# Kernel tuning notes

Hardware: AMD Instinct MI355X
Metric: run time of the kernel (lower is better)

Reference implementation:

```python
import jax, jax.numpy as jnp
import numpy as np

NUM_HEADS = 16
HEAD_DIM = 64
MAX_TIME = 10000


def apply_rope(x):
    """Interleaved RoPE, faithful to apply_rotary_encoding with the _rope_kernel.

    The NxN kernel maps pairs (x0, x1) -> (-x1, x0); we do it with a reshape
    instead of the dense matmul for efficiency (same math).
    x: [b, t, h, d]
    """
    b, t, h, d = x.shape
    pos = jnp.arange(t, dtype=jnp.float32)                         # [t]
    freq_seq = jnp.arange(d // 2, dtype=jnp.float32) / (d // 2)
    inv_freq = jnp.repeat(jnp.float32(MAX_TIME) ** (-freq_seq), 2)  # [d], interleaved
    theta = pos[:, None] * inv_freq[None, :]                        # [t, d]
    pairs = x.reshape(b, t, h, d // 2, 2)
    x_rot = jnp.stack([-pairs[..., 1], pairs[..., 0]], axis=-1).reshape(b, t, h, d)
    cos = jnp.cos(theta).astype(x.dtype)[None, :, None, :]
    sin = jnp.sin(theta).astype(x.dtype)[None, :, None, :]
    return x * cos + x_rot * sin


def setup_inputs() -> dict:
    key = jax.random.key(0)
    ks = jax.random.split(key, 6)
    B, T, E = 8, 1024, 1024
    H = NUM_HEADS * HEAD_DIM
    s = 0.02  # typical init scale for bias-free Linear weights
    return {
        "inputs_q": jax.random.normal(ks[0], (B, T, E), jnp.float32),
        "inputs_kv": jax.random.normal(ks[1], (B, T, E), jnp.float32),
        "w_q": jax.random.normal(ks[2], (E, H), jnp.float32) * s,
        "w_k": jax.random.normal(ks[3], (E, H), jnp.float32) * s,
        "w_v": jax.random.normal(ks[4], (E, H), jnp.float32) * s,
        "w_o": jax.random.normal(ks[5], (H, E), jnp.float32) * s,
    }


def reference(inputs_q, inputs_kv, w_q, w_k, w_v, w_o):
    b, t, e = inputs_q.shape
    q = (inputs_q @ w_q).reshape(b, t, NUM_HEADS, HEAD_DIM)   # [b,t,h,d]
    k = (inputs_kv @ w_k).reshape(b, -1, NUM_HEADS, HEAD_DIM)  # [b,T,h,d]
    v = (inputs_kv @ w_v).reshape(b, -1, NUM_HEADS, HEAD_DIM)
    q = apply_rope(q)
    k = apply_rope(k)
    logits = jnp.einsum('bthd,bThd->bhtT', q, k) * (1.0 / jnp.sqrt(jnp.float32(HEAD_DIM)))
    attn = jax.nn.softmax(logits, axis=-1)                    # [b,h,t,T]
    out = jnp.einsum('bhtT,bThd->bthd', attn, v).reshape(b, t, NUM_HEADS * HEAD_DIM)
    return out @ w_o                                          # [b,t,e]
```

## Files before the change

### kernel.cpp

```cpp
#include <hip/hip_runtime.h>
#include <math.h>


typedef __attribute__((ext_vector_type(8))) short bf16x8;
typedef __attribute__((ext_vector_type(4))) float f32x4;
typedef __attribute__((ext_vector_type(16))) float f32x16;

#define LOG2E 1.44269504f
#define QSCALE (0.125f * LOG2E)

__device__ __forceinline__ ushort f2bf(float f) {
    union { float f; uint32_t u; } v; v.f = f;
    uint32_t r = (v.u + 0x7FFF + ((v.u >> 16) & 1)) >> 16;
    return (ushort)r;
}
__device__ __forceinline__ uint cvt_pk_bf16(float a, float b) {
    uint r;
    asm("v_cvt_pk_bf16_f32 %0, %1, %2" : "=v"(r) : "v"(a), "v"(b));
    return r;
}
__device__ __forceinline__ float bf2f(ushort u) {
    union { uint32_t u; float f; } v; v.u = ((uint32_t)u) << 16;
    return v.f;
}

__device__ __forceinline__ void gload16(const ushort* g, ushort* l) {
    __builtin_amdgcn_global_load_lds(
        (const __attribute__((address_space(1))) unsigned int*)g,
        (__attribute__((address_space(3))) unsigned int*)l, 16, 0, 0);
}

__global__ void build_rope_tbl(float2* __restrict__ tbl)
{
    int idx = blockIdx.x * 256 + threadIdx.x;
    int t = idx >> 5, i = idx & 31;
    float inv_freq = exp2f(-(float)i * (13.28771238f / 32.0f));
    float s, c;
    sincosf((float)t * inv_freq, &s, &c);
    tbl[idx] = make_float2(c, s);
}

__global__ void cast_bf16_2(const float* __restrict__ X0, ushort* __restrict__ Y0,
                            const float* __restrict__ X1, ushort* __restrict__ Y1)
{
    const float* X = blockIdx.y ? X1 : X0;
    ushort* Y = blockIdx.y ? Y1 : Y0;
    int i = blockIdx.x * 256 + threadIdx.x;
    float4 a = ((const float4*)X)[2 * i];
    float4 b = ((const float4*)X)[2 * i + 1];
    union { float4 f; ushort u[8]; } o;
    o.u[0] = f2bf(a.x); o.u[1] = f2bf(a.y); o.u[2] = f2bf(a.z); o.u[3] = f2bf(a.w);
    o.u[4] = f2bf(b.x); o.u[5] = f2bf(b.y); o.u[6] = f2bf(b.z); o.u[7] = f2bf(b.w);
    ((float4*)Y)[i] = o.f;
}

__global__ void transpose_cast_4(const float* __restrict__ w0, ushort* __restrict__ t0,
                                 const float* __restrict__ w1, ushort* __restrict__ t1,
                                 const float* __restrict__ w2, ushort* __restrict__ t2,
                                 const float* __restrict__ w3, ushort* __restrict__ t3)
{
    const int z = blockIdx.z;
    const float* W = (z == 0) ? w0 : (z == 1) ? w1 : (z == 2) ? w2 : w3;
    ushort* Wt = (z == 0) ? t0 : (z == 1) ? t1 : (z == 2) ? t2 : t3;
    __shared__ float t[32][33];
    int bx = blockIdx.x * 32, by = blockIdx.y * 32;
    int tx = threadIdx.x, ty = threadIdx.y;
#pragma unroll
    for (int e = 0; e < 32; e += 8)
        t[ty + e][tx] = W[(size_t)(by + ty + e) * 1024 + bx + tx];
    __syncthreads();
#pragma unroll
    for (int e = 0; e < 32; e += 8)
        Wt[(size_t)(bx + ty + e) * 1024 + by + tx] = f2bf(t[tx][ty + e]);
}

__global__ __launch_bounds__(256, 4)
void gemm_qkv(const ushort* __restrict__ Aq, const ushort* __restrict__ Akv,
              const ushort* __restrict__ Wt, ushort* __restrict__ Out,
              const float2* __restrict__ tbl)
{
    const int K = 1024, N = 1024;
    __shared__ ushort As[2][128 * 32];
    __shared__ ushort Bs[2][128 * 32];
    const int tid = threadIdx.x;
    const int w = tid >> 6, l = tid & 63;
    const int mat = blockIdx.y >> 3;
    const int row0 = blockIdx.x * 128, col0 = (blockIdx.y & 7) * 128;
    const int wr = (w >> 1) * 64, wc = (w & 1) * 64;

    const ushort* A = mat ? Akv : Aq;
    const ushort* Bt = Wt + (size_t)mat * (1024 * 1024);
    ushort* C = Out + (size_t)mat * 8388608;

    f32x4 acc[4][4];
#pragma unroll
    for (int i = 0; i < 4; ++i)
#pragma unroll
        for (int j = 0; j < 4; ++j) acc[i][j] = (f32x4)0.f;

    const ushort* Ag = A + (size_t)(row0 + w * 32 + (l >> 2)) * K + (l & 3) * 8;
    const ushort* Bg = Bt + (size_t)(col0 + w * 32 + (l >> 2)) * K + (l & 3) * 8;

    const int arow = (wr + (l & 15)) * 32;
    const int brow = (wc + (l & 15)) * 32;
    const int koff = (l >> 4) * 8;

    auto STAGE = [&](int buf, int kt) {
        ushort* Asw = &As[buf][w * 1024];
        ushort* Bsw = &Bs[buf][w * 1024];
        gload16(Ag + kt, Asw);
        gload16(Ag + 16 * K + kt, Asw + 512);
        gload16(Bg + kt, Bsw);
        gload16(Bg + 16 * K + kt, Bsw + 512);
    };
    auto COMPUTE = [&](int buf) {
        bf16x8 af[4], bfr[4];
#pragma unroll
        for (int fm = 0; fm < 4; ++fm)
            af[fm] = *(const bf16x8*)&As[buf][arow + fm * 512 + koff];
#pragma unroll
        for (int fn = 0; fn < 4; ++fn)
            bfr[fn] = *(const bf16x8*)&Bs[buf][brow + fn * 512 + koff];
#pragma unroll
        for (int fm = 0; fm < 4; ++fm)
#pragma unroll
            for (int fn = 0; fn < 4; ++fn)
                acc[fm][fn] = __builtin_amdgcn_mfma_f32_16x16x32_bf16(
                    af[fm], bfr[fn], acc[fm][fn], 0, 0, 0);
    };

    STAGE(0, 0);
    asm volatile("s_waitcnt vmcnt(0)" ::: "memory");
    __builtin_amdgcn_s_barrier();
    int cur = 0;
    for (int kt = 32; kt < K; kt += 32) {
        STAGE(cur ^ 1, kt);
        COMPUTE(cur);
        asm volatile("s_waitcnt vmcnt(0)" ::: "memory");
        __builtin_amdgcn_s_barrier();
        cur ^= 1;
    }
    COMPUTE(cur);

    const int crow = (l >> 4) * 4;
    const int ccol = l & 15;

    if (mat < 2) {
        const float scale = (mat == 0) ? QSCALE : 1.0f;
        const int odd = ccol & 1;
        int ipair[4];
#pragma unroll
        for (int fn = 0; fn < 4; ++fn)
            ipair[fn] = (fn * 16 + ccol) >> 1;
#pragma unroll
        for (int fm = 0; fm < 4; ++fm)
#pragma unroll
            for (int r = 0; r < 4; ++r) {
                int t = (row0 + wr + fm * 16 + crow + r) & 1023;
                const float2* tb = tbl + (t << 5);
#pragma unroll
                for (int fn = 0; fn < 4; ++fn) {
                    float x = acc[fm][fn][r];
                    float partner = __shfl_xor(x, 1, 64);
                    float2 cs = tb[ipair[fn]];
                    float o = odd ? fmaf(partner, cs.y, x * cs.x)
                                  : fmaf(-partner, cs.y, x * cs.x);
                    acc[fm][fn][r] = o * scale;
                }
            }
    }

#pragma unroll
    for (int fm = 0; fm < 4; ++fm)
#pragma unroll
        for (int fn = 0; fn < 4; ++fn)
#pragma unroll
            for (int r = 0; r < 4; ++r) {
                size_t row = row0 + wr + fm * 16 + crow + r;
                size_t col = col0 + wc + fn * 16 + ccol;
                C[row * N + col] = f2bf(acc[fm][fn][r]);
            }
}

__global__ __launch_bounds__(256, 2)
void gemm_out(const ushort* __restrict__ A, const ushort* __restrict__ Bt,
              float* __restrict__ C, int M, int N, int K)
{
    __shared__ ushort As[2][128 * 32];
    __shared__ ushort Bs[2][128 * 32];
    const int tid = threadIdx.x;
    const int w = tid >> 6, l = tid & 63;
    const int row0 = blockIdx.x * 128, col0 = blockIdx.y * 128;
    const int wr = (w >> 1) * 64, wc = (w & 1) * 64;

    f32x4 acc[4][4];
#pragma unroll
    for (int i = 0; i < 4; ++i)
#pragma unroll
        for (int j = 0; j < 4; ++j) acc[i][j] = (f32x4)0.f;

    const ushort* Ag = A + (size_t)(row0 + w * 32 + (l >> 2)) * K + (l & 3) * 8;
    const ushort* Bg = Bt + (size_t)(col0 + w * 32 + (l >> 2)) * K + (l & 3) * 8;

    const int arow = (wr + (l & 15)) * 32;
    const int brow = (wc + (l & 15)) * 32;
    const int koff = (l >> 4) * 8;

    auto STAGE = [&](int buf, int kt) {
        ushort* Asw = &As[buf][w * 1024];
        ushort* Bsw = &Bs[buf][w * 1024];
        gload16(Ag + kt, Asw);
        gload16(Ag + 16 * K + kt, Asw + 512);
        gload16(Bg + kt, Bsw);
        gload16(Bg + 16 * K + kt, Bsw + 512);
    };
    auto COMPUTE = [&](int buf) {
        bf16x8 af[4], bfr[4];
#pragma unroll
        for (int fm = 0; fm < 4; ++fm)
            af[fm] = *(const bf16x8*)&As[buf][arow + fm * 512 + koff];
#pragma unroll
        for (int fn = 0; fn < 4; ++fn)
            bfr[fn] = *(const bf16x8*)&Bs[buf][brow + fn * 512 + koff];
#pragma unroll
        for (int fm = 0; fm < 4; ++fm)
#pragma unroll
            for (int fn = 0; fn < 4; ++fn)
                acc[fm][fn] = __builtin_amdgcn_mfma_f32_16x16x32_bf16(
                    af[fm], bfr[fn], acc[fm][fn], 0, 0, 0);
    };

    STAGE(0, 0);
    asm volatile("s_waitcnt vmcnt(0)" ::: "memory");
    __builtin_amdgcn_s_barrier();
    int cur = 0;
    for (int kt = 32; kt < K; kt += 32) {
        STAGE(cur ^ 1, kt);
        COMPUTE(cur);
        asm volatile("s_waitcnt vmcnt(0)" ::: "memory");
        __builtin_amdgcn_s_barrier();
        cur ^= 1;
    }
    COMPUTE(cur);

    const int crow = (l >> 4) * 4;
    const int ccol = l & 15;
#pragma unroll
    for (int fm = 0; fm < 4; ++fm)
#pragma unroll
        for (int fn = 0; fn < 4; ++fn)
#pragma unroll
            for (int r = 0; r < 4; ++r) {
                size_t row = row0 + wr + fm * 16 + crow + r;
                size_t col = col0 + wc + fn * 16 + ccol;
                C[row * N + col] = acc[fm][fn][r];
            }
}

__global__ __launch_bounds__(256, 4)
void attn_bf16_v2(const ushort* __restrict__ Q, const ushort* __restrict__ K,
                  const ushort* __restrict__ V, ushort* __restrict__ O)
{
    __shared__ uint Ksu[64 * 34];
    __shared__ uint Vtu[64 * 34];
    __shared__ uint Os[4][32 * 36];

    const int tid = threadIdx.x;
    const int w = tid >> 6, l = tid & 63;
    const int lo = l & 31, hi = l >> 5;
    const int bid = blockIdx.x;
    const int qt = bid >> 7;
    const int hb = bid & 127;
    const int h = hb >> 3, b = hb & 7;
    const int colh = h * 64;

    const size_t qrow = (size_t)(b * 1024 + qt * 128 + w * 32 + lo);
    bf16x8 qb[4];
#pragma unroll
    for (int kc = 0; kc < 4; ++kc)
        qb[kc] = *(const bf16x8*)&Q[qrow * 1024 + colh + kc * 16 + hi * 8];

    f32x16 acc[2];
#pragma unroll
    for (int i = 0; i < 2; ++i) acc[i] = (f32x16)0.f;
    float lsum = 0.f;

    const size_t kvbase = (size_t)b * 1024 * 1024 + colh;

    const int skey = tid >> 3, sc = tid & 7;
    const int kp = tid & 31, vg = tid >> 5;

    for (int kt = 0; kt < 16; ++kt) {
        __syncthreads();
#pragma unroll
        for (int u = 0; u < 2; ++u) {
            int key = skey + u * 32;
            uint4 kv = *(const uint4*)&K[kvbase + (size_t)(kt * 64 + key) * 1024 + sc * 8];
            *(uint2*)&Ksu[key * 34 + sc * 4] = make_uint2(kv.x, kv.y);
            *(uint2*)&Ksu[key * 34 + sc * 4 + 2] = make_uint2(kv.z, kv.w);
        }
        {
            uint4 va = *(const uint4*)&V[kvbase + (size_t)(kt * 64 + 2 * kp) * 1024 + vg * 8];
            uint4 vb = *(const uint4*)&V[kvbase + (size_t)(kt * 64 + 2 * kp + 1) * 1024 + vg * 8];
            const ushort* pa = (const ushort*)&va;
            const ushort* pb = (const ushort*)&vb;
#pragma unroll
            for (int e = 0; e < 8; ++e)
                Vtu[(vg * 8 + e) * 34 + kp] = (uint)pa[e] | ((uint)pb[e] << 16);
        }
        __syncthreads();

        uint pw[16];
#pragma unroll
        for (int mt = 0; mt < 2; ++mt) {
            f32x16 s = (f32x16)0.f;
            const int rbase = (mt * 32 + lo) * 34 + hi * 4;
#pragma unroll
            for (int kc = 0; kc < 4; ++kc) {
                union { uint2 d[2]; bf16x8 v; } ak;
                ak.d[0] = *(const uint2*)&Ksu[rbase + kc * 8];
                ak.d[1] = *(const uint2*)&Ksu[rbase + kc * 8 + 2];
                s = __builtin_amdgcn_mfma_f32_32x32x16_bf16(ak.v, qb[kc], s, 0, 0, 0);
            }
            float p[16];
#pragma unroll
            for (int r = 0; r < 16; ++r) {
                p[r] = exp2f(s[r]);
                lsum += p[r];
            }
#pragma unroll
            for (int rp = 0; rp < 8; ++rp)
                pw[mt * 8 + rp] = cvt_pk_bf16(p[2 * rp], p[2 * rp + 1]);
        }

        bf16x8 pf[4];
#pragma unroll
        for (int mt = 0; mt < 2; ++mt) {
            uint* W = &pw[mt * 8];
            uint e0 = (uint)__shfl_xor((int)(hi ? W[0] : W[2]), 32);
            uint e1 = (uint)__shfl_xor((int)(hi ? W[1] : W[3]), 32);
            uint e2 = (uint)__shfl_xor((int)(hi ? W[4] : W[6]), 32);
            uint e3 = (uint)__shfl_xor((int)(hi ? W[5] : W[7]), 32);
            union { uint u[4]; bf16x8 v; } f0, f1;
            if (hi == 0) {
                f0.u[0] = W[0]; f0.u[1] = W[1]; f0.u[2] = e0; f0.u[3] = e1;
                f1.u[0] = W[4]; f1.u[1] = W[5]; f1.u[2] = e2; f1.u[3] = e3;
            } else {
                f0.u[0] = e0; f0.u[1] = e1; f0.u[2] = W[2]; f0.u[3] = W[3];
                f1.u[0] = e2; f1.u[1] = e3; f1.u[2] = W[6]; f1.u[3] = W[7];
            }
            pf[mt * 2 + 0] = f0.v;
            pf[mt * 2 + 1] = f1.v;
        }

#pragma unroll
        for (int dmt = 0; dmt < 2; ++dmt) {
            const int rbase = (dmt * 32 + lo) * 34 + hi * 4;
#pragma unroll
            for (int kcg = 0; kcg < 4; ++kcg) {
                union { uint2 d[2]; bf16x8 v; } vk;
                vk.d[0] = *(const uint2*)&Vtu[rbase + kcg * 8];
                vk.d[1] = *(const uint2*)&Vtu[rbase + kcg * 8 + 2];
                acc[dmt] = __builtin_amdgcn_mfma_f32_32x32x16_bf16(vk.v, pf[kcg], acc[dmt], 0, 0, 0);
            }
        }
    }

    float tot = lsum + __shfl_xor(lsum, 32);
    float inv = 1.0f / tot;

    uint* Osw = &Os[w][0];
#pragma unroll
    for (int dmt = 0; dmt < 2; ++dmt)
#pragma unroll
        for (int rp = 0; rp < 8; ++rp) {
            float a0 = acc[dmt][2 * rp] * inv;
            float a1 = acc[dmt][2 * rp + 1] * inv;
            Osw[lo * 36 + dmt * 16 + (rp & 1) + 4 * (rp >> 1) + 2 * hi] =
                cvt_pk_bf16(a0, a1);
        }
    __builtin_amdgcn_s_waitcnt(0);
#pragma unroll
    for (int u = 0; u < 4; ++u) {
        int slot = l + u * 64;
        int qr = slot >> 3, c = slot & 7;
        float4 val = *(const float4*)&Osw[qr * 36 + c * 4];
        *(float4*)&O[(size_t)(b * 1024 + qt * 128 + w * 32 + qr) * 1024 + colh + c * 8] = val;
    }
}

extern "C" void kernel_launch(void* const* d_in, const int* in_sizes, int n_in,
                              void* d_out, int out_size, void* d_ws, size_t ws_size,
                              hipStream_t stream)
{
    const float* xq  = (const float*)d_in[0];
    const float* xkv = (const float*)d_in[1];
    const float* wq  = (const float*)d_in[2];
    const float* wk  = (const float*)d_in[3];
    const float* wv  = (const float*)d_in[4];
    const float* wo  = (const float*)d_in[5];
    float* out = (float*)d_out;

    const int M = 8192, N = 1024, Kd = 1024;
    ushort* Aq  = (ushort*)d_ws;
    ushort* Akv = Aq  + 8388608;
    ushort* WqT = Akv + 8388608;
    ushort* WkT = WqT + 1048576;
    ushort* WvT = WkT + 1048576;
    ushort* WoT = WvT + 1048576;
    ushort* Qb  = WoT + 1048576;
    ushort* Kb  = Qb  + 8388608;
    ushort* Vb  = Kb  + 8388608;
    ushort* Ob  = Vb  + 8388608;
    float2* Tbl = (float2*)(Ob + 8388608);

    build_rope_tbl<<<128, 256, 0, stream>>>(Tbl);
    cast_bf16_2<<<dim3(4096, 2), 256, 0, stream>>>(xq, Aq, xkv, Akv);
    transpose_cast_4<<<dim3(32, 32, 4), dim3(32, 8), 0, stream>>>(
        wq, WqT, wk, WkT, wv, WvT, wo, WoT);

    gemm_qkv<<<dim3(64, 24), 256, 0, stream>>>(Aq, Akv, WqT, Qb, Tbl);

    attn_bf16_v2<<<1024, 256, 0, stream>>>(Qb, Kb, Vb, Ob);

    gemm_out<<<dim3(64, 8), 256, 0, stream>>>(Ob, WoT, out, M, N, Kd);
}
```

Baseline: 185.1 us.

## Rewrite QKV GEMM as 256x256 eight-wave kernel with swizzled LDS pipeline

Replaces the 128x128 four-wave QKV projection GEMM with a 256x256 tile, 512-thread kernel that uses a 64-wide K step, XOR-swizzled LDS layout, and fine-grained interleaving of global-to-LDS loads, LDS reads and MFMA phases under explicit barriers and priority hints. Blocks are remapped for locality across the 384 tiles. The aim is more operand reuse per LDS byte, fewer bank conflicts and better overlap of memory traffic with matrix math. In exchange it uses 128 KB of LDS and many more accumulator registers, which limits occupancy, and the hand-scheduled waitcnt and barrier sequence is fragile.

```diff
diff --git a/kernel.cpp b/kernel.cpp
--- a/kernel.cpp
+++ b/kernel.cpp
@@ -8,6 +8,10 @@
 
 #define LOG2E 1.44269504f
 #define QSCALE (0.125f * LOG2E)
+
+#define SCHED0 __builtin_amdgcn_sched_barrier(0)
+#define SBAR   do { SCHED0; __builtin_amdgcn_s_barrier(); SCHED0; } while (0)
+#define WAITVM(N) do { asm volatile("s_waitcnt vmcnt(" #N ")" ::: "memory"); SCHED0; } while (0)
 
 __device__ __forceinline__ ushort f2bf(float f) {
     union { float f; uint32_t u; } v; v.f = f;
@@ -74,73 +78,123 @@
         Wt[(size_t)(bx + ty + e) * 1024 + by + tx] = f2bf(t[tx][ty + e]);
 }
 
-__global__ __launch_bounds__(256, 4)
-void gemm_qkv(const ushort* __restrict__ Aq, const ushort* __restrict__ Akv,
-              const ushort* __restrict__ Wt, ushort* __restrict__ Out,
-              const float2* __restrict__ tbl)
-{
-    const int K = 1024, N = 1024;
-    __shared__ ushort As[2][128 * 32];
-    __shared__ ushort Bs[2][128 * 32];
+__global__ __launch_bounds__(512, 2)
+void gemm_qkv8(const ushort* __restrict__ Aq, const ushort* __restrict__ Akv,
+               const ushort* __restrict__ Wt, ushort* __restrict__ Out,
+               const float2* __restrict__ tbl)
+{
+    __shared__ ushort lds[65536];
+
     const int tid = threadIdx.x;
-    const int w = tid >> 6, l = tid & 63;
-    const int mat = blockIdx.y >> 3;
-    const int row0 = blockIdx.x * 128, col0 = (blockIdx.y & 7) * 128;
-    const int wr = (w >> 1) * 64, wc = (w & 1) * 64;
-
-    const ushort* A = mat ? Akv : Aq;
-    const ushort* Bt = Wt + (size_t)mat * (1024 * 1024);
+    const int wid = tid >> 6, l = tid & 63;
+    const int wr = wid >> 2, wc = wid & 3;
+
+    const int id = (blockIdx.x & 7) * 48 + (blockIdx.x >> 3);
+    const int g = id >> 5;
+    const int rt = id & 31;
+    const int mat = g >> 2, ct = g & 3;
+    const int row0 = rt * 256, col0 = ct * 256;
+
+    const ushort* A  = mat ? Akv : Aq;
+    const ushort* Bt = Wt + (size_t)mat * 1048576;
     ushort* C = Out + (size_t)mat * 8388608;
 
-    f32x4 acc[4][4];
-#pragma unroll
-    for (int i = 0; i < 4; ++i)
+    const int srow = tid >> 3;
+    const int scol = ((tid & 7) ^ ((tid >> 3) & 7)) * 8;
+    const ushort* Abase = A  + (size_t)(row0 + srow) * 1024 + scol;
+    const ushort* Bbase = Bt + (size_t)(col0 + srow) * 1024 + scol;
+
+    auto STG_A = [&](int t, int h) {
+        const ushort* s = Abase + h * 131072 + t * 64;
+        ushort* d = &lds[(t & 1) * 16384 + h * 8192 + tid * 8];
+        gload16(s, d);
+        gload16(s + 65536, d + 4096);
+    };
+    auto STG_B = [&](int t, int h) {
+        const ushort* s = Bbase + h * 131072 + t * 64;
+        ushort* d = &lds[32768 + (t & 1) * 16384 + h * 8192 + tid * 8];
+        gload16(s, d);
+        gload16(s + 65536, d + 4096);
+    };
+
+    const int lrow = l & 15;
+    const int rc0 = ((((l >> 4) * 16)      ^ ((l & 7) << 4)) >> 1);
+    const int rc1 = (((64 + (l >> 4) * 16) ^ ((l & 7) << 4)) >> 1);
+    const int abase = wr * 8192 + lrow * 64;
+    const int bbase = 32768 + (wc >> 1) * 8192 + (wc & 1) * 4096 + lrow * 64;
+
+    bf16x8 aK0[8], aK1[8], bK0[4], bK1[4];
+    f32x4 acc[8][4];
+#pragma unroll
+    for (int i = 0; i < 8; ++i)
 #pragma unroll
         for (int j = 0; j < 4; ++j) acc[i][j] = (f32x4)0.f;
 
-    const ushort* Ag = A + (size_t)(row0 + w * 32 + (l >> 2)) * K + (l & 3) * 8;
-    const ushort* Bg = Bt + (size_t)(col0 + w * 32 + (l >> 2)) * K + (l & 3) * 8;
-
-    const int arow = (wr + (l & 15)) * 32;
-    const int brow = (wc + (l & 15)) * 32;
-    const int koff = (l >> 4) * 8;
-
-    auto STAGE = [&](int buf, int kt) {
-        ushort* Asw = &As[buf][w * 1024];
-        ushort* Bsw = &Bs[buf][w * 1024];
-        gload16(Ag + kt, Asw);
-        gload16(Ag + 16 * K + kt, Asw + 512);
-        gload16(Bg + kt, Bsw);
-        gload16(Bg + 16 * K + kt, Bsw + 512);
-    };
-    auto COMPUTE = [&](int buf) {
-        bf16x8 af[4], bfr[4];
+    auto RDA = [&](bf16x8* dst, int d, int rc) {
+#pragma unroll
+        for (int fm = 0; fm < 8; ++fm)
+            dst[fm] = *(const bf16x8*)&lds[d * 16384 + abase + fm * 1024 + rc];
+    };
+    auto RDB = [&](bf16x8* dst, int d, int rc) {
+#pragma unroll
+        for (int fn = 0; fn < 4; ++fn)
+            dst[fn] = *(const bf16x8*)&lds[d * 16384 + bbase + fn * 1024 + rc];
+    };
+    auto MFMAH = [&](const bf16x8* a, const bf16x8* b, int h) {
+        __builtin_amdgcn_s_setprio(1);
 #pragma unroll
         for (int fm = 0; fm < 4; ++fm)
-            af[fm] = *(const bf16x8*)&As[buf][arow + fm * 512 + koff];
-#pragma unroll
-        for (int fn = 0; fn < 4; ++fn)
-            bfr[fn] = *(const bf16x8*)&Bs[buf][brow + fn * 512 + koff];
-#pragma unroll
-        for (int fm = 0; fm < 4; ++fm)
 #pragma unroll
             for (int fn = 0; fn < 4; ++fn)
-                acc[fm][fn] = __builtin_amdgcn_mfma_f32_16x16x32_bf16(
-                    af[fm], bfr[fn], acc[fm][fn], 0, 0, 0);
-    };
-
-    STAGE(0, 0);
-    asm volatile("s_waitcnt vmcnt(0)" ::: "memory");
-    __builtin_amdgcn_s_barrier();
-    int cur = 0;
-    for (int kt = 32; kt < K; kt += 32) {
-        STAGE(cur ^ 1, kt);
-        COMPUTE(cur);
-        asm volatile("s_waitcnt vmcnt(0)" ::: "memory");
-        __builtin_amdgcn_s_barrier();
-        cur ^= 1;
+                acc[h * 4 + fm][fn] = __builtin_amdgcn_mfma_f32_16x16x32_bf16(
+                    a[h * 4 + fm], b[fn], acc[h * 4 + fm][fn], 0, 0, 0);
+        __builtin_amdgcn_s_setprio(0);
+    };
+
+    STG_A(0, 0); STG_A(0, 1); STG_B(0, 0); STG_B(0, 1);
+    STG_A(1, 0); STG_A(1, 1);
+    WAITVM(4);
+    SBAR;
+
+#pragma unroll 1
+    for (int I = 0; I < 8; ++I) {
+        const int t0 = 2 * I, t1 = t0 + 1;
+        const bool full = (I < 7);
+        RDA(aK0, 0, rc0); RDB(bK0, 0, rc0);
+        STG_B(t1, 0);
+        MFMAH(aK0, bK0, 0);
+        SBAR;
+        RDA(aK1, 0, rc1);
+        STG_B(t1, 1);
+        MFMAH(aK0, bK0, 1);
+        SBAR;
+        RDB(bK1, 0, rc1);
+        if (full) STG_A(t0 + 2, 0);
+        MFMAH(aK1, bK1, 0);
+        SBAR;
+        if (full) STG_A(t0 + 2, 1);
+        MFMAH(aK1, bK1, 1);
+        if (full) { WAITVM(4); } else { WAITVM(0); }
+        SBAR;
+        RDA(aK0, 1, rc0); RDB(bK0, 1, rc0);
+        if (full) STG_B(t0 + 2, 0);
+        MFMAH(aK0, bK0, 0);
+        SBAR;
+        RDA(aK1, 1, rc1);
+        if (full) STG_B(t0 + 2, 1);
+        MFMAH(aK0, bK0, 1);
+        SBAR;
+        RDB(bK1, 1, rc1);
+        if (full) STG_A(t1 + 2, 0);
+        MFMAH(aK1, bK1, 0);
+        SBAR;
+        MFMAH(aK1, bK1, 1);
+        if (full) {
+            STG_A(t1 + 2, 1);
+            WAITVM(4);
+        }
+        SBAR;
     }
-    COMPUTE(cur);
 
     const int crow = (l >> 4) * 4;
     const int ccol = l & 15;
@@ -153,10 +207,10 @@
         for (int fn = 0; fn < 4; ++fn)
             ipair[fn] = (fn * 16 + ccol) >> 1;
 #pragma unroll
-        for (int fm = 0; fm < 4; ++fm)
+        for (int fm = 0; fm < 8; ++fm)
 #pragma unroll
             for (int r = 0; r < 4; ++r) {
-                int t = (row0 + wr + fm * 16 + crow + r) & 1023;
+                int t = (row0 + wr * 128 + fm * 16 + crow + r) & 1023;
                 const float2* tb = tbl + (t << 5);
 #pragma unroll
                 for (int fn = 0; fn < 4; ++fn) {
@@ -171,14 +225,14 @@
     }
 
 #pragma unroll
-    for (int fm = 0; fm < 4; ++fm)
+    for (int fm = 0; fm < 8; ++fm)
 #pragma unroll
         for (int fn = 0; fn < 4; ++fn)
 #pragma unroll
             for (int r = 0; r < 4; ++r) {
-                size_t row = row0 + wr + fm * 16 + crow + r;
-                size_t col = col0 + wc + fn * 16 + ccol;
-                C[row * N + col] = f2bf(acc[fm][fn][r]);
+                size_t row = row0 + wr * 128 + fm * 16 + crow + r;
+                size_t col = col0 + wc * 64 + fn * 16 + ccol;
+                C[row * 1024 + col] = f2bf(acc[fm][fn][r]);
             }
 }
 
@@ -419,7 +473,7 @@
     transpose_cast_4<<<dim3(32, 32, 4), dim3(32, 8), 0, stream>>>(
         wq, WqT, wk, WkT, wv, WvT, wo, WoT);
 
-    gemm_qkv<<<dim3(64, 24), 256, 0, stream>>>(Aq, Akv, WqT, Qb, Tbl);
+    gemm_qkv8<<<384, 512, 0, stream>>>(Aq, Akv, WqT, Qb, Tbl);
 
     attn_bf16_v2<<<1024, 256, 0, stream>>>(Qb, Kb, Vb, Ob);
 
```

New measurement: 199.8 us. 8.0% more time.
